# Performance work log

Hardware: AMD Instinct MI355X
Metric: run time of the kernel (lower is better)

## Reference

```python
import jax, jax.numpy as jnp
import numpy as np

N = 50000      # nodes
E = 800000     # edges
D = 128        # hidden dim (args.dim) == num_features
B = 5          # GIN blocks
G = 512        # graphs in batch
C = 10         # classes
EPS_GIN = 128.0  # GINConv(nn, in_channels) -> eps = in_channels = 128 (faithful to source)
BN_EPS = 1e-5


def setup_inputs() -> dict:
    key = jax.random.key(0)
    ks = jax.random.split(key, 12)
    xav = 0.1  # ~xavier_uniform std for 128x128
    x = jax.random.normal(ks[0], (N, D), jnp.float32)
    edge_index = jax.random.randint(ks[1], (2, E), 0, N, dtype=jnp.int64)
    batch = jax.random.randint(ks[2], (N,), 0, G, dtype=jnp.int64)
    return dict(
        x=x, edge_index=edge_index, batch=batch,
        W1=jax.random.normal(ks[3], (B, D, D), jnp.float32) * xav,
        b1=jnp.zeros((B, D), jnp.float32),
        g1=jnp.ones((B, D), jnp.float32),
        be1=jnp.zeros((B, D), jnp.float32),
        W2=jax.random.normal(ks[4], (B, D, D), jnp.float32) * xav,
        b2=jnp.zeros((B, D), jnp.float32),
        g2=jnp.ones((B, D), jnp.float32),
        be2=jnp.zeros((B, D), jnp.float32),
        bn_g=jnp.ones((B * D,), jnp.float32),
        bn_b=jnp.zeros((B * D,), jnp.float32),
        Wc1=jax.random.normal(ks[5], (B * D, D), jnp.float32) * 0.05,
        bc1=jnp.zeros((D,), jnp.float32),
        Wc2=jax.random.normal(ks[6], (D, C), jnp.float32) * 0.1,
        bc2=jnp.zeros((C,), jnp.float32),
    )


def _bn(h, g, b):
    # training-mode BatchNorm1d: biased variance over the batch (node/graph) dim
    mu = h.mean(axis=0)
    var = h.var(axis=0)
    return g * (h - mu) * jax.lax.rsqrt(var + BN_EPS) + b


def reference(x, edge_index, batch, W1, b1, g1, be1, W2, b2, g2, be2,
              bn_g, bn_b, Wc1, bc1, Wc2, bc2):
    src, dst = edge_index[0], edge_index[1]
    feats = []
    for i in range(B):
        # GIN aggregation: out[dst] += x[src]
        agg = jax.ops.segment_sum(x[src], dst, num_segments=N)   # [N, D]
        h = (1.0 + EPS_GIN) * x + agg
        h = _bn(jax.nn.relu(h @ W1[i] + b1[i]), g1[i], be1[i])
        h = _bn(jax.nn.relu(h @ W2[i] + b2[i]), g2[i], be2[i])
        x = h
        # global_add_pool per graph
        feats.append(jax.ops.segment_sum(x, batch, num_segments=G))  # [G, D]
    f = jnp.concatenate(feats, axis=1)          # [G, B*D]
    f = _bn(f, bn_g, bn_b)
    f = jax.nn.relu(f @ Wc1 + bc1)              # dropout p=0 (eval)
    logits = f @ Wc2 + bc2                      # [G, C]
    return jax.nn.log_softmax(logits, axis=-1)
```

## Files before the change

kernel.cpp:

```cpp
#include <hip/hip_runtime.h>
#include <hip/hip_bf16.h>

#define NN 50000
#define NE 800000
#define DD 128
#define NB 5
#define NG 512
#define NC 10
#define BN_EPS 1e-5f
#define EPS1 129.0f
#define GATHER_BLOCKS 12500

typedef __hip_bfloat16 bf16;
typedef __attribute__((ext_vector_type(8))) short short8;
typedef __attribute__((ext_vector_type(4))) float f32x4;

__device__ __forceinline__ float b2f(const bf16 v) { return __bfloat162float(v); }
__device__ __forceinline__ float us2f(unsigned int s) {
    return __uint_as_float((s & 0xffffu) << 16);
}
__device__ __forceinline__ unsigned pack2(float a, float b) {
    union { bf16 h; unsigned short u; } ua, ub;
    ua.h = __float2bfloat16(a); ub.h = __float2bfloat16(b);
    return ((unsigned)ub.u << 16) | (unsigned)ua.u;
}
__device__ __forceinline__ short f2bfs(float f) {
    union { bf16 h; short s; } u; u.h = __float2bfloat16(f); return u.s;
}

#define OFF_AGGH   0
#define OFF_XF     3200000
#define OFF_H1     6400000
#define OFF_FEATS  9600000
#define OFF_CSA    9927680
#define OFF_CSB    9927936
#define OFF_SC6    9928192
#define OFF_SH6    9928832
#define OFF_FLAGS  9929472
#define OFF_PARAMS 9929480
#define OFF_DEG    10055680
#define OFF_OFFS   10105680
#define OFF_ELIST  10155712
#define OFF_BDEG   10955712
#define OFF_BOFFS  10956224
#define OFF_RANK   10956800
#define OFF_PART   11006800

#define P_W1T  0
#define P_W2T  81920
#define P_WC1  163840
#define P_B1   245760
#define P_G1   246400
#define P_BE1  247040
#define P_B2   247680
#define P_G2   248320
#define P_BE2  248960
#define P_BNG  249600
#define P_BNB  250240
#define P_BC1  250880
#define P_WC2  251008
#define P_BC2  252288

struct SmallSrc { const void* s[11]; };

__global__ void k_detect(const unsigned* __restrict__ xw, const int* __restrict__ eiw,
                         const int* __restrict__ bw, int* flags, int* __restrict__ bdeg) {
    __shared__ int sh[3];
    const int t = threadIdx.x;
    bdeg[t] = 0; bdeg[256 + t] = 0;
    if (t < 3) sh[t] = 0;
    __syncthreads();
    int c = 0;
    for (int i = 0; i < 16; i++) {
        unsigned w = xw[t * 16 + i];
        unsigned e = (w >> 7) & 0xff;
        c += (e >= 110 && e <= 131) ? 1 : 0;
    }
    atomicAdd(&sh[0], c);
    atomicAdd(&sh[1], (eiw[2 * t + 1] != 0) ? 1 : 0);
    atomicAdd(&sh[2], (bw[2 * t + 1] != 0) ? 1 : 0);
    __syncthreads();
    if (t == 0) {
        flags[0] = (sh[0] > 2048) ? 1 : 0;
        flags[1] = (sh[1] < 8) ? 1 : 0;
        flags[2] = (sh[2] < 8) ? 1 : 0;
    }
}

__global__ void k_bhist(const int* __restrict__ flags, const int* __restrict__ batch,
                        int* __restrict__ bdeg, int* __restrict__ deg) {
    int n = blockIdx.x * 256 + threadIdx.x;
    if (n >= NN) return;
    deg[n] = 0;
    int g = flags[2] ? batch[2 * n] : batch[n];
    atomicAdd(&bdeg[g], 1);
}

__launch_bounds__(512)
__global__ void k_bscan(int* __restrict__ bdeg, int* __restrict__ boffs) {
    __shared__ int part[512];
    const int t = threadIdx.x;
    int d0 = bdeg[t];
    part[t] = d0;
    __syncthreads();
    for (int d = 1; d < 512; d <<= 1) {
        int v = (t >= d) ? part[t - d] : 0;
        __syncthreads();
        part[t] += v;
        __syncthreads();
    }
    int ex = part[t] - d0;
    boffs[t] = ex;
    bdeg[t] = ex;
    if (t == 511) boffs[512] = part[511];
}

__global__ void k_bplace(const int* __restrict__ flags, const int* __restrict__ batch,
                         int* __restrict__ bcur, int* __restrict__ rank) {
    int n = blockIdx.x * 256 + threadIdx.x;
    if (n >= NN) return;
    int g = flags[2] ? batch[2 * n] : batch[n];
    rank[n] = atomicAdd(&bcur[g], 1);
}

__global__ void k_convert_x(const int* __restrict__ flags, const void* __restrict__ xr,
                            const int* __restrict__ rank, bf16* __restrict__ xfh) {
    int i = blockIdx.x * 256 + threadIdx.x;
    int r = i >> 4, seg = i & 15;
    uint4 o;
    if (flags[0]) {
        o = ((const uint4*)xr)[i];
    } else {
        float4 a = ((const float4*)xr)[2 * i], b = ((const float4*)xr)[2 * i + 1];
        o.x = pack2(a.x, a.y); o.y = pack2(a.z, a.w);
        o.z = pack2(b.x, b.y); o.w = pack2(b.z, b.w);
    }
    ((uint4*)xfh)[(long)rank[r] * 16 + seg] = o;
}

__global__ void k_convert_params(const int* __restrict__ flags, const void* w1,
                                 const void* w2, const void* wc1, SmallSrc srcs,
                                 bf16* __restrict__ pb) {
    int i = blockIdx.x * 256 + threadIdx.x;
    if (i < 245760) {
        int which = i / 81920, j = i % 81920;
        const void* src = (which == 0) ? w1 : (which == 1) ? w2 : wc1;
        float v = flags[0] ? us2f(((const unsigned short*)src)[j]) : ((const float*)src)[j];
        if (which == 2) {
            pb[P_WC1 + j] = __float2bfloat16(v);
        } else {
            int layer = j >> 14, rem = j & 16383;
            int k = rem >> 7, c = rem & 127;
            bf16* dst = pb + (which == 0 ? P_W1T : P_W2T);
            dst[(layer << 14) + c * DD + k] = __float2bfloat16(v);
        }
    } else {
        int j = i - 245760;
        if (j >= 6538) return;
        int seg, off;
        if (j < 5120)      { seg = j / 640; off = j - seg * 640; }
        else if (j < 5248) { seg = 8;  off = j - 5120; }
        else if (j < 6528) { seg = 9;  off = j - 5248; }
        else               { seg = 10; off = j - 6528; }
        const void* s = srcs.s[seg];
        float v = flags[0] ? us2f(((const unsigned short*)s)[off]) : ((const float*)s)[off];
        pb[P_B1 + j] = __float2bfloat16(v);
    }
}

__global__ void k_hist(const int* __restrict__ flags, const int* __restrict__ ei,
                       const int* __restrict__ rank, int* __restrict__ deg) {
    int e = blockIdx.x * 256 + threadIdx.x;
    int d = flags[1] ? ei[2 * NE + 2 * e] : ei[NE + e];
    atomicAdd(&deg[rank[d]], 1);
}

__global__ void k_scan_part(const int* __restrict__ deg, int* __restrict__ part) {
    __shared__ int red[256];
    const int b = blockIdx.x, t = threadIdx.x;
    int i0 = b * 1024 + t * 4;
    int s = 0;
    if (i0 + 3 < NN) {
        int4 v = *(const int4*)(deg + i0);
        s = v.x + v.y + v.z + v.w;
    } else {
        for (int k = 0; k < 4; k++) if (i0 + k < NN) s += deg[i0 + k];
    }
    red[t] = s;
    __syncthreads();
    for (int d = 128; d > 0; d >>= 1) {
        if (t < d) red[t] += red[t + d];
        __syncthreads();
    }
    if (t == 0) part[b] = red[0];
}

__global__ void k_scan_apply(int* __restrict__ deg, const int* __restrict__ part,
                             int* __restrict__ offs) {
    __shared__ int red[256];
    __shared__ int base_sh, total_sh;
    const int b = blockIdx.x, t = threadIdx.x;
    if (t < 64) {
        int v = (t < 49) ? part[t] : 0;
        int s = v;
        for (int d = 1; d < 64; d <<= 1) {
            int x = __shfl_up(s, d);
            if (t >= d) s += x;
        }
        if (t == b)  base_sh = s - v;
        if (t == 48) total_sh = s;
    }
    int i0 = b * 1024 + t * 4;
    int v[4]; int s = 0;
    #pragma unroll
    for (int k = 0; k < 4; k++) {
        int idx = i0 + k;
        v[k] = (idx < NN) ? deg[idx] : 0;
        s += v[k];
    }
    red[t] = s;
    __syncthreads();
    for (int d = 1; d < 256; d <<= 1) {
        int x = (t >= d) ? red[t - d] : 0;
        __syncthreads();
        red[t] += x;
        __syncthreads();
    }
    if (b == 0 && t == 0) offs[NN] = total_sh;
    int pre = base_sh + ((t == 0) ? 0 : red[t - 1]);
    #pragma unroll
    for (int k = 0; k < 4; k++) {
        int idx = i0 + k;
        if (idx < NN) { offs[idx] = pre; deg[idx] = pre; pre += v[k]; }
    }
}

__global__ void k_place(const int* __restrict__ flags, const int* __restrict__ ei,
                        const int* __restrict__ rank, int* __restrict__ curs,
                        int* __restrict__ elist) {
    int e = blockIdx.x * 256 + threadIdx.x;
    int s, d;
    if (flags[1]) { s = ei[2 * e]; d = ei[2 * NE + 2 * e]; }
    else          { s = ei[e];     d = ei[NE + e]; }
    elist[atomicAdd(&curs[rank[d]], 1)] = rank[s];
}

__device__ __forceinline__ void pool_body(int g, int t, const bf16* __restrict__ xfh,
                                          const int* __restrict__ boffs,
                                          const float* __restrict__ csB,
                                          const bf16* __restrict__ g2,
                                          const bf16* __restrict__ be2,
                                          float* __restrict__ feats_blk) {
    __shared__ float2 red[3][64];
    const int l = t & 63;
    const int h = t >> 6;
    const int lo = boffs[g], hi = boffs[g + 1];
    const unsigned* xw = (const unsigned*)xfh;
    float s0 = 0.f, s1 = 0.f;
    for (int n = lo + h; n < hi; n += 4) {
        unsigned p = xw[(long)n * 64 + l];
        s0 += us2f(p); s1 += us2f(p >> 16);
    }
    if (h) red[h - 1][l] = make_float2(s0, s1);
    __syncthreads();
    if (h == 0) {
        s0 += red[0][l].x + red[1][l].x + red[2][l].x;
        s1 += red[0][l].y + red[1][l].y + red[2][l].y;
        int c = l * 2;
        float mu0 = csB[c] * (1.f / NN);
        float var0 = csB[128 + c] * (1.f / NN) - mu0 * mu0;
        float sc0 = b2f(g2[c]) * rsqrtf(var0 + BN_EPS);
        float sh0 = b2f(be2[c]) - mu0 * sc0;
        float mu1 = csB[c + 1] * (1.f / NN);
        float var1 = csB[128 + c + 1] * (1.f / NN) - mu1 * mu1;
        float sc1 = b2f(g2[c + 1]) * rsqrtf(var1 + BN_EPS);
        float sh1 = b2f(be2[c + 1]) - mu1 * sc1;
        float cnt = (float)(hi - lo);
        float* fp = feats_blk + (long)g * (NB * DD) + c;
        fp[0] = sc0 * s0 + cnt * sh0;
        fp[1] = sc1 * s1 + cnt * sh1;
    }
}

__global__ void k_gather_pool(const int* __restrict__ offs, const int* __restrict__ elist,
                              const bf16* __restrict__ xfh, bf16* __restrict__ aggh,
                              const float* __restrict__ csB, const bf16* __restrict__ g2,
                              const bf16* __restrict__ be2, float* __restrict__ csA_zero,
                              const int* __restrict__ boffs, float* __restrict__ feats_prev) {
    if (blockIdx.x >= GATHER_BLOCKS) {
        if (feats_prev)
            pool_body(blockIdx.x - GATHER_BLOCKS, threadIdx.x, xfh, boffs,
                      csB, g2, be2, feats_prev);
        return;
    }
    if (blockIdx.x == 0) csA_zero[threadIdx.x] = 0.f;
    const int w = threadIdx.x >> 6;
    const int lane = threadIdx.x & 63;
    const int n = blockIdx.x * 4 + w;
    const int base = offs[n], end = offs[n + 1];
    const unsigned* xw = (const unsigned*)xfh;
    unsigned sp = xw[(long)n * 64 + lane];
    float ax = EPS1 * us2f(sp), ay = EPS1 * us2f(sp >> 16);
    for (int i = base; i < end; i += 64) {
        int cnt = min(64, end - i);
        int e = (i + lane < end) ? elist[i + lane] : 0;
        int j = 0;
        for (; j + 16 <= cnt; j += 16) {
            unsigned p[16];
            #pragma unroll
            for (int q = 0; q < 16; q++) {
                int sj = __shfl(e, j + q);
                p[q] = xw[(long)sj * 64 + lane];
            }
            #pragma unroll
            for (int q = 0; q < 16; q++) {
                ax += us2f(p[q]); ay += us2f(p[q] >> 16);
            }
        }
        for (; j + 8 <= cnt; j += 8) {
            unsigned p[8];
            #pragma unroll
            for (int q = 0; q < 8; q++) {
                int sj = __shfl(e, j + q);
                p[q] = xw[(long)sj * 64 + lane];
            }
            #pragma unroll
            for (int q = 0; q < 8; q++) {
                ax += us2f(p[q]); ay += us2f(p[q] >> 16);
            }
        }
        for (; j < cnt; j++) {
            int sj = __shfl(e, j);
            unsigned p = xw[(long)sj * 64 + lane];
            ax += us2f(p); ay += us2f(p >> 16);
        }
    }
    if (csB) {
        int c = lane * 2;
        float fac = (float)(end - base) + EPS1;
        float mu0 = csB[c] * (1.f / NN);
        float var0 = csB[128 + c] * (1.f / NN) - mu0 * mu0;
        float sc0 = b2f(g2[c]) * rsqrtf(var0 + BN_EPS);
        float sh0 = b2f(be2[c]) - mu0 * sc0;
        float mu1 = csB[c + 1] * (1.f / NN);
        float var1 = csB[128 + c + 1] * (1.f / NN) - mu1 * mu1;
        float sc1 = b2f(g2[c + 1]) * rsqrtf(var1 + BN_EPS);
        float sh1 = b2f(be2[c + 1]) - mu1 * sc1;
        ax = sc0 * ax + fac * sh0;
        ay = sc1 * ay + fac * sh1;
    }
    ((unsigned*)aggh)[(long)n * 64 + lane] = pack2(ax, ay);
}

__launch_bounds__(256)
__global__ void k_pool(const bf16* __restrict__ xfh, const int* __restrict__ boffs,
                       const float* __restrict__ csB, const bf16* __restrict__ g2,
                       const bf16* __restrict__ be2, float* __restrict__ feats_blk) {
    pool_body(blockIdx.x, threadIdx.x, xfh, boffs, csB, g2, be2, feats_blk);
}

#define WS_S 136
__launch_bounds__(512)
__global__ void k_gemm_mfma(const bf16* __restrict__ A, const bf16* __restrict__ WT,
                            const bf16* __restrict__ bias,
                            const float* __restrict__ bn_cs, const bf16* __restrict__ bn_g,
                            const bf16* __restrict__ bn_be,
                            bf16* __restrict__ Out, float* __restrict__ cs_out,
                            float* cs_zero) {
    __shared__ short Ws[128 * WS_S];
    __shared__ float s_cs[256];
    __shared__ float s_sc[DD], s_sh[DD];
    const int t = threadIdx.x;
    const int row0 = blockIdx.x * 128;

    if (t < 256) {
        if (cs_zero && blockIdx.x == 0) cs_zero[t] = 0.f;
        s_cs[t] = 0.f;
    }
    if (bn_cs && t < DD) {
        float mu = bn_cs[t] * (1.f / NN);
        float var = bn_cs[128 + t] * (1.f / NN) - mu * mu;
        float sc = b2f(bn_g[t]) * rsqrtf(var + BN_EPS);
        s_sc[t] = sc;
        s_sh[t] = b2f(bn_be[t]) - mu * sc;
    }
    {
        const uint4* Wg = (const uint4*)WT;
        #pragma unroll
        for (int i = 0; i < 4; i++) {
            int idx = i * 512 + t;
            int row = idx >> 4, seg = idx & 15;
            *(uint4*)(&Ws[row * WS_S + seg * 8]) = Wg[idx];
        }
    }
    __syncthreads();

    const int w = t >> 6;
    const int lane = t & 63;
    const int m = lane & 15;
    const int half = lane >> 4;
    const int r = row0 + w * 16 + m;

    short8 afrag[4];
    if (r < NN) {
        #pragma unroll
        for (int kk = 0; kk < 4; kk++)
            afrag[kk] = *(const short8*)(A + (long)r * DD + kk * 32 + half * 8);
        if (bn_cs) {
            #pragma unroll
            for (int kk = 0; kk < 4; kk++) {
                int c0 = kk * 32 + half * 8;
                uint4 p = *(uint4*)&afrag[kk];
                float v0 = us2f(p.x) * s_sc[c0+0] + s_sh[c0+0];
                float v1 = us2f(p.x >> 16) * s_sc[c0+1] + s_sh[c0+1];
                float v2 = us2f(p.y) * s_sc[c0+2] + s_sh[c0+2];
                float v3 = us2f(p.y >> 16) * s_sc[c0+3] + s_sh[c0+3];
                float v4 = us2f(p.z) * s_sc[c0+4] + s_sh[c0+4];
                float v5 = us2f(p.z >> 16) * s_sc[c0+5] + s_sh[c0+5];
                float v6 = us2f(p.w) * s_sc[c0+6] + s_sh[c0+6];
                float v7 = us2f(p.w >> 16) * s_sc[c0+7] + s_sh[c0+7];
                p.x = pack2(v0, v1); p.y = pack2(v2, v3);
                p.z = pack2(v4, v5); p.w = pack2(v6, v7);
                afrag[kk] = *(short8*)&p;
            }
        }
    } else {
        #pragma unroll
        for (int kk = 0; kk < 4; kk++) afrag[kk] = (short8){0,0,0,0,0,0,0,0};
    }

    f32x4 acc[8];
    #pragma unroll
    for (int nt = 0; nt < 8; nt++) acc[nt] = (f32x4){0.f, 0.f, 0.f, 0.f};

    #pragma unroll
    for (int nt = 0; nt < 8; nt++) {
        const short* wrow = &Ws[(nt * 16 + m) * WS_S + half * 8];
        #pragma unroll
        for (int kk = 0; kk < 4; kk++) {
            short8 b = *(const short8*)(wrow + kk * 32);
            acc[nt] = __builtin_amdgcn_mfma_f32_16x16x32_bf16(afrag[kk], b, acc[nt], 0, 0, 0);
        }
    }

    __syncthreads();
    short* Cs = Ws;
    #pragma unroll
    for (int nt = 0; nt < 8; nt++) {
        int col = nt * 16 + m;
        float bi = b2f(bias[col]);
        float ps = 0.f, pq = 0.f;
        #pragma unroll
        for (int reg = 0; reg < 4; reg++) {
            int rr = row0 + w * 16 + half * 4 + reg;
            float o = fmaxf(acc[nt][reg] + bi, 0.f);
            Cs[(w * 16 + half * 4 + reg) * WS_S + col] = f2bfs(o);
            if (rr < NN) { ps += o; pq += o * o; }
        }
        ps += __shfl_xor(ps, 16); ps += __shfl_xor(ps, 32);
        pq += __shfl_xor(pq, 16); pq += __shfl_xor(pq, 32);
        if (half == 0) {
            atomicAdd(&s_cs[col], ps);
            atomicAdd(&s_cs[128 + col], pq);
        }
    }
    __syncthreads();
    #pragma unroll
    for (int i = 0; i < 4; i++) {
        int idx = i * 512 + t;
        int row = idx >> 4, seg = idx & 15;
        int rr = row0 + row;
        if (rr < NN)
            *(uint4*)(Out + (long)rr * DD + seg * 8) = *(uint4*)(&Cs[row * WS_S + seg * 8]);
    }
    if (t < 256) atomicAdd(&cs_out[t], s_cs[t]);
}

__global__ void k_feat_stats(const float* __restrict__ feats, const bf16* __restrict__ bn_g,
                             const bf16* __restrict__ bn_b, float* __restrict__ sc6,
                             float* __restrict__ sh6) {
    int j = blockIdx.x * 256 + threadIdx.x;
    if (j >= NB * DD) return;
    float s = 0.f, sq = 0.f;
    for (int g = 0; g < NG; g++) {
        float v = feats[(long)g * (NB * DD) + j];
        s += v; sq += v * v;
    }
    float mu = s / NG;
    float var = sq / NG - mu * mu;
    float sc = b2f(bn_g[j]) * rsqrtf(var + BN_EPS);
    sc6[j] = sc;
    sh6[j] = b2f(bn_b[j]) - mu * sc;
}

__launch_bounds__(128)
__global__ void k_head(const int* __restrict__ flags, const float* __restrict__ feats,
                       const float* __restrict__ sc6, const float* __restrict__ sh6,
                       const bf16* __restrict__ Wc1, const bf16* __restrict__ bc1,
                       const bf16* __restrict__ Wc2, const bf16* __restrict__ bc2,
                       void* out) {
    __shared__ float fs[NB * DD];
    __shared__ float f1[DD];
    __shared__ float lg[NC + 2];
    const int g = blockIdx.x, t = threadIdx.x;
    for (int j = t; j < NB * DD; j += 128)
        fs[j] = feats[(long)g * (NB * DD) + j] * sc6[j] + sh6[j];
    __syncthreads();
    float acc = b2f(bc1[t]);
    for (int j = 0; j < NB * DD; j++) acc += fs[j] * b2f(Wc1[j * DD + t]);
    f1[t] = fmaxf(acc, 0.f);
    __syncthreads();
    if (t < NC) {
        float a = b2f(bc2[t]);
        for (int k = 0; k < DD; k++) a += f1[k] * b2f(Wc2[k * NC + t]);
        lg[t] = a;
    }
    __syncthreads();
    if (t == 0) {
        float m = -1e30f;
        for (int c = 0; c < NC; c++) m = fmaxf(m, lg[c]);
        float s = 0.f;
        for (int c = 0; c < NC; c++) s += expf(lg[c] - m);
        lg[NC] = m + logf(s);
    }
    __syncthreads();
    if (t < NC) {
        float val = lg[t] - lg[NC];
        if (flags[0]) ((bf16*)out)[g * NC + t] = __float2bfloat16(val);
        else          ((float*)out)[g * NC + t] = val;
    }
}

extern "C" void kernel_launch(void* const* d_in, const int* in_sizes, int n_in,
                              void* d_out, int out_size, void* d_ws, size_t ws_size,
                              hipStream_t stream) {
    const void* x     = d_in[0];
    const int*  ei    = (const int*)d_in[1];
    const int*  batch = (const int*)d_in[2];

    float* ws    = (float*)d_ws;
    bf16*  aggh  = (bf16*)(ws + OFF_AGGH);
    bf16*  xfh   = (bf16*)(ws + OFF_XF);
    bf16*  h1h   = (bf16*)(ws + OFF_H1);
    float* feats = ws + OFF_FEATS;
    float* csA   = ws + OFF_CSA;
    float* csB   = ws + OFF_CSB;
    float* sc6   = ws + OFF_SC6;
    float* sh6   = ws + OFF_SH6;
    int*   flags = (int*)(ws + OFF_FLAGS);
    bf16*  pb    = (bf16*)(ws + OFF_PARAMS);
    int*   deg   = (int*)(ws + OFF_DEG);
    int*   offs  = (int*)(ws + OFF_OFFS);
    int*   elist = (int*)(ws + OFF_ELIST);
    int*   bdeg  = (int*)(ws + OFF_BDEG);
    int*   boffs = (int*)(ws + OFF_BOFFS);
    int*   rank  = (int*)(ws + OFF_RANK);
    int*   part  = (int*)(ws + OFF_PART);

    bf16 *pW1T = pb + P_W1T, *pW2T = pb + P_W2T, *pWc1 = pb + P_WC1;
    bf16 *pb1 = pb + P_B1, *pg1 = pb + P_G1, *pbe1 = pb + P_BE1;
    bf16 *pb2 = pb + P_B2, *pg2 = pb + P_G2, *pbe2 = pb + P_BE2;
    bf16 *pbng = pb + P_BNG, *pbnb = pb + P_BNB;
    bf16 *pbc1 = pb + P_BC1, *pWc2 = pb + P_WC2, *pbc2 = pb + P_BC2;

    k_detect<<<1, 256, 0, stream>>>((const unsigned*)x, ei, batch, flags, bdeg);

    k_bhist<<<(NN + 255) / 256, 256, 0, stream>>>(flags, batch, bdeg, deg);
    k_bscan<<<1, 512, 0, stream>>>(bdeg, boffs);
    k_bplace<<<(NN + 255) / 256, 256, 0, stream>>>(flags, batch, bdeg, rank);

    k_convert_x<<<NN * DD / 8 / 256, 256, 0, stream>>>(flags, x, rank, xfh);

    SmallSrc ss;
    ss.s[0] = d_in[4];  ss.s[1] = d_in[5];  ss.s[2] = d_in[6];
    ss.s[3] = d_in[8];  ss.s[4] = d_in[9];  ss.s[5] = d_in[10];
    ss.s[6] = d_in[11]; ss.s[7] = d_in[12];
    ss.s[8] = d_in[14]; ss.s[9] = d_in[15]; ss.s[10] = d_in[16];
    k_convert_params<<<(245760 + 6538 + 255) / 256, 256, 0, stream>>>(
        flags, d_in[3], d_in[7], d_in[13], ss, pb);

    k_hist<<<NE / 256, 256, 0, stream>>>(flags, ei, rank, deg);
    k_scan_part<<<49, 256, 0, stream>>>(deg, part);
    k_scan_apply<<<49, 256, 0, stream>>>(deg, part, offs);
    k_place<<<NE / 256, 256, 0, stream>>>(flags, ei, rank, deg, elist);

    const int gemm_blocks = (NN + 127) / 128;
    for (int i = 0; i < NB; i++) {
        k_gather_pool<<<GATHER_BLOCKS + NG, 256, 0, stream>>>(
            offs, elist, xfh, aggh,
            (i == 0) ? nullptr : csB,
            pg2 + (i - 1) * DD, pbe2 + (i - 1) * DD, csA,
            boffs, (i == 0) ? nullptr : feats + (i - 1) * DD);
        k_gemm_mfma<<<gemm_blocks, 512, 0, stream>>>(aggh, pW1T + i * DD * DD, pb1 + i * DD,
                                                     nullptr, nullptr, nullptr,
                                                     h1h, csA, csB);
        k_gemm_mfma<<<gemm_blocks, 512, 0, stream>>>(h1h, pW2T + i * DD * DD, pb2 + i * DD,
                                                     csA, pg1 + i * DD, pbe1 + i * DD,
                                                     xfh, csB, nullptr);
    }
    k_pool<<<NG, 256, 0, stream>>>(xfh, boffs, csB, pg2 + (NB - 1) * DD,
                                   pbe2 + (NB - 1) * DD, feats + (NB - 1) * DD);

    k_feat_stats<<<3, 256, 0, stream>>>(feats, pbng, pbnb, sc6, sh6);
    k_head<<<NG, 128, 0, stream>>>(flags, feats, sc6, sh6, pWc1, pbc1, pWc2, pbc2, d_out);
}
```

Before: 685.2 us.

## Fuse GEMM pair and tail kernels using grid-wide software barriers

Merges the two per-block GEMM launches into one persistent kernel of 512 blocks that synchronizes on a global atomic barrier between the two layers. The final pool, feature-stats and head kernels are merged the same way, and the edge histogram is folded into the x-convert launch. The aim is to cut kernel launch gaps and drain/fill overhead. In exchange it relies on all 512 blocks being co-resident; if they are not, the spin barrier deadlocks.

```diff
diff --git a/kernel.cpp b/kernel.cpp
--- a/kernel.cpp
+++ b/kernel.cpp
@@ -10,6 +10,8 @@
 #define BN_EPS 1e-5f
 #define EPS1 129.0f
 #define GATHER_BLOCKS 12500
+#define GP_BLOCKS 512
+#define GEMM_TILES 391
 
 typedef __hip_bfloat16 bf16;
 typedef __attribute__((ext_vector_type(8))) short short8;
@@ -26,6 +28,22 @@
 }
 __device__ __forceinline__ short f2bfs(float f) {
     union { bf16 h; short s; } u; u.h = __float2bfloat16(f); return u.s;
+}
+
+__device__ __forceinline__ void gbar(int* cnt, int* gen, int nb) {
+    __syncthreads();
+    if (threadIdx.x == 0) {
+        __threadfence();
+        int g = atomicAdd(gen, 0);
+        if (atomicAdd(cnt, 1) == nb - 1) {
+            atomicExch(cnt, 0);
+            atomicAdd(gen, 1);
+        } else {
+            while (atomicAdd(gen, 0) == g) __builtin_amdgcn_s_sleep(2);
+        }
+        __threadfence();
+    }
+    __syncthreads();
 }
 
 #define OFF_AGGH   0
@@ -45,6 +63,7 @@
 #define OFF_BOFFS  10956224
 #define OFF_RANK   10956800
 #define OFF_PART   11006800
+#define OFF_BAR    11006864
 
 #define P_W1T  0
 #define P_W2T  81920
@@ -97,9 +116,11 @@
 }
 
 __launch_bounds__(512)
-__global__ void k_bscan(int* __restrict__ bdeg, int* __restrict__ boffs) {
+__global__ void k_bscan(int* __restrict__ bdeg, int* __restrict__ boffs,
+                        int* __restrict__ barst) {
     __shared__ int part[512];
     const int t = threadIdx.x;
+    if (t < 4) barst[t] = 0;
     int d0 = bdeg[t];
     part[t] = d0;
     __syncthreads();
@@ -123,8 +144,15 @@
     rank[n] = atomicAdd(&bcur[g], 1);
 }
 
-__global__ void k_convert_x(const int* __restrict__ flags, const void* __restrict__ xr,
-                            const int* __restrict__ rank, bf16* __restrict__ xfh) {
+__global__ void k_convert_hist(const int* __restrict__ flags, const void* __restrict__ xr,
+                               const int* __restrict__ rank, bf16* __restrict__ xfh,
+                               const int* __restrict__ ei, int* __restrict__ deg) {
+    if (blockIdx.x >= 3125) {
+        int e = (blockIdx.x - 3125) * 256 + threadIdx.x;
+        int d = flags[1] ? ei[2 * NE + 2 * e] : ei[NE + e];
+        atomicAdd(&deg[rank[d]], 1);
+        return;
+    }
     int i = blockIdx.x * 256 + threadIdx.x;
     int r = i >> 4, seg = i & 15;
     uint4 o;
@@ -166,13 +194,6 @@
         float v = flags[0] ? us2f(((const unsigned short*)s)[off]) : ((const float*)s)[off];
         pb[P_B1 + j] = __float2bfloat16(v);
     }
-}
-
-__global__ void k_hist(const int* __restrict__ flags, const int* __restrict__ ei,
-                       const int* __restrict__ rank, int* __restrict__ deg) {
-    int e = blockIdx.x * 256 + threadIdx.x;
-    int d = flags[1] ? ei[2 * NE + 2 * e] : ei[NE + e];
-    atomicAdd(&deg[rank[d]], 1);
 }
 
 __global__ void k_scan_part(const int* __restrict__ deg, int* __restrict__ part) {
@@ -280,6 +301,7 @@
         fp[0] = sc0 * s0 + cnt * sh0;
         fp[1] = sc1 * s1 + cnt * sh1;
     }
+    __syncthreads();
 }
 
 __global__ void k_gather_pool(const int* __restrict__ offs, const int* __restrict__ elist,
@@ -352,38 +374,17 @@
     ((unsigned*)aggh)[(long)n * 64 + lane] = pack2(ax, ay);
 }
 
-__launch_bounds__(256)
-__global__ void k_pool(const bf16* __restrict__ xfh, const int* __restrict__ boffs,
-                       const float* __restrict__ csB, const bf16* __restrict__ g2,
-                       const bf16* __restrict__ be2, float* __restrict__ feats_blk) {
-    pool_body(blockIdx.x, threadIdx.x, xfh, boffs, csB, g2, be2, feats_blk);
-}
-
 #define WS_S 136
-__launch_bounds__(512)
-__global__ void k_gemm_mfma(const bf16* __restrict__ A, const bf16* __restrict__ WT,
-                            const bf16* __restrict__ bias,
-                            const float* __restrict__ bn_cs, const bf16* __restrict__ bn_g,
-                            const bf16* __restrict__ bn_be,
-                            bf16* __restrict__ Out, float* __restrict__ cs_out,
-                            float* cs_zero) {
-    __shared__ short Ws[128 * WS_S];
-    __shared__ float s_cs[256];
-    __shared__ float s_sc[DD], s_sh[DD];
-    const int t = threadIdx.x;
-    const int row0 = blockIdx.x * 128;
-
-    if (t < 256) {
-        if (cs_zero && blockIdx.x == 0) cs_zero[t] = 0.f;
-        s_cs[t] = 0.f;
-    }
-    if (bn_cs && t < DD) {
-        float mu = bn_cs[t] * (1.f / NN);
-        float var = bn_cs[128 + t] * (1.f / NN) - mu * mu;
-        float sc = b2f(bn_g[t]) * rsqrtf(var + BN_EPS);
-        s_sc[t] = sc;
-        s_sh[t] = b2f(bn_be[t]) - mu * sc;
-    }
+__device__ __forceinline__ void gemm_tile(const bf16* __restrict__ A,
+                                          const bf16* __restrict__ WT,
+                                          const bf16* __restrict__ bias,
+                                          const float* __restrict__ s_sc,
+                                          const float* __restrict__ s_sh, bool do_bn,
+                                          bf16* __restrict__ Out,
+                                          float* __restrict__ cs_out,
+                                          short* Ws, float* s_cs, int tile, int t) {
+    const int row0 = tile * 128;
+    if (t < 256) s_cs[t] = 0.f;
     {
         const uint4* Wg = (const uint4*)WT;
         #pragma unroll
@@ -406,7 +407,7 @@
         #pragma unroll
         for (int kk = 0; kk < 4; kk++)
             afrag[kk] = *(const short8*)(A + (long)r * DD + kk * 32 + half * 8);
-        if (bn_cs) {
+        if (do_bn) {
             #pragma unroll
             for (int kk = 0; kk < 4; kk++) {
                 int c0 = kk * 32 + half * 8;
@@ -474,41 +475,87 @@
             *(uint4*)(Out + (long)rr * DD + seg * 8) = *(uint4*)(&Cs[row * WS_S + seg * 8]);
     }
     if (t < 256) atomicAdd(&cs_out[t], s_cs[t]);
-}
-
-__global__ void k_feat_stats(const float* __restrict__ feats, const bf16* __restrict__ bn_g,
-                             const bf16* __restrict__ bn_b, float* __restrict__ sc6,
-                             float* __restrict__ sh6) {
-    int j = blockIdx.x * 256 + threadIdx.x;
-    if (j >= NB * DD) return;
-    float s = 0.f, sq = 0.f;
-    for (int g = 0; g < NG; g++) {
-        float v = feats[(long)g * (NB * DD) + j];
-        s += v; sq += v * v;
-    }
-    float mu = s / NG;
-    float var = sq / NG - mu * mu;
-    float sc = b2f(bn_g[j]) * rsqrtf(var + BN_EPS);
-    sc6[j] = sc;
-    sh6[j] = b2f(bn_b[j]) - mu * sc;
-}
-
-__launch_bounds__(128)
-__global__ void k_head(const int* __restrict__ flags, const float* __restrict__ feats,
-                       const float* __restrict__ sc6, const float* __restrict__ sh6,
+    __syncthreads();
+}
+
+__launch_bounds__(512)
+__global__ void k_gemm_pair(const bf16* __restrict__ aggh, bf16* __restrict__ h1h,
+                            bf16* __restrict__ xfh,
+                            const bf16* __restrict__ W1T, const bf16* __restrict__ b1,
+                            const bf16* __restrict__ W2T, const bf16* __restrict__ b2,
+                            const bf16* __restrict__ g1, const bf16* __restrict__ be1,
+                            float* __restrict__ csA, float* __restrict__ csB,
+                            int* __restrict__ barst) {
+    __shared__ short Ws[128 * WS_S];
+    __shared__ float s_cs[256];
+    __shared__ float s_sc[DD], s_sh[DD];
+    const int t = threadIdx.x;
+    const int bid = blockIdx.x;
+
+    if (bid == 400 && t < 256) csB[t] = 0.f;
+    if (bid < GEMM_TILES)
+        gemm_tile(aggh, W1T, b1, nullptr, nullptr, false, h1h, csA, Ws, s_cs, bid, t);
+
+    gbar(&barst[0], &barst[1], GP_BLOCKS);
+
+    if (t < DD) {
+        float mu = csA[t] * (1.f / NN);
+        float var = csA[128 + t] * (1.f / NN) - mu * mu;
+        float sc = b2f(g1[t]) * rsqrtf(var + BN_EPS);
+        s_sc[t] = sc;
+        s_sh[t] = b2f(be1[t]) - mu * sc;
+    }
+    __syncthreads();
+    if (bid < GEMM_TILES)
+        gemm_tile(h1h, W2T, b2, s_sc, s_sh, true, xfh, csB, Ws, s_cs, bid, t);
+}
+
+__launch_bounds__(256)
+__global__ void k_tail(const int* __restrict__ flags, const bf16* __restrict__ xfh,
+                       const int* __restrict__ boffs, const float* __restrict__ csB,
+                       const bf16* __restrict__ g2, const bf16* __restrict__ be2,
+                       float* __restrict__ feats, const bf16* __restrict__ bn_g,
+                       const bf16* __restrict__ bn_b, float* __restrict__ sc6,
+                       float* __restrict__ sh6,
                        const bf16* __restrict__ Wc1, const bf16* __restrict__ bc1,
                        const bf16* __restrict__ Wc2, const bf16* __restrict__ bc2,
-                       void* out) {
+                       void* out, int* __restrict__ barst) {
+    const int t = threadIdx.x, bid = blockIdx.x;
+
+    pool_body(bid, t, xfh, boffs, csB, g2, be2, feats + (NB - 1) * DD);
+
+    gbar(&barst[2], &barst[3], GP_BLOCKS);
+
+    {
+        int j = bid * 256 + t;
+        if (j < NB * DD) {
+            float s = 0.f, sq = 0.f;
+            for (int g = 0; g < NG; g++) {
+                float v = feats[(long)g * (NB * DD) + j];
+                s += v; sq += v * v;
+            }
+            float mu = s / NG;
+            float var = sq / NG - mu * mu;
+            float sc = b2f(bn_g[j]) * rsqrtf(var + BN_EPS);
+            sc6[j] = sc;
+            sh6[j] = b2f(bn_b[j]) - mu * sc;
+        }
+    }
+
+    gbar(&barst[2], &barst[3], GP_BLOCKS);
+
     __shared__ float fs[NB * DD];
     __shared__ float f1[DD];
     __shared__ float lg[NC + 2];
-    const int g = blockIdx.x, t = threadIdx.x;
-    for (int j = t; j < NB * DD; j += 128)
+    const int g = bid;
+    for (int j = t; j < NB * DD; j += 256)
         fs[j] = feats[(long)g * (NB * DD) + j] * sc6[j] + sh6[j];
     __syncthreads();
-    float acc = b2f(bc1[t]);
-    for (int j = 0; j < NB * DD; j++) acc += fs[j] * b2f(Wc1[j * DD + t]);
-    f1[t] = fmaxf(acc, 0.f);
+    if (t < DD) {
+        float acc = b2f(bc1[t]);
+        for (int j = 0; j < NB * DD; j++) acc += fs[j] * b2f(Wc1[j * DD + t]);
+        f1[t] = fmaxf(acc, 0.f);
+    }
     __syncthreads();
     if (t < NC) {
         float a = b2f(bc2[t]);
@@ -556,6 +603,7 @@
     int*   boffs = (int*)(ws + OFF_BOFFS);
     int*   rank  = (int*)(ws + OFF_RANK);
     int*   part  = (int*)(ws + OFF_PART);
+    int*   barst = (int*)(ws + OFF_BAR);
 
     bf16 *pW1T = pb + P_W1T, *pW2T = pb + P_W2T, *pWc1 = pb + P_WC1;
     bf16 *pb1 = pb + P_B1, *pg1 = pb + P_G1, *pbe1 = pb + P_BE1;
@@ -564,12 +612,11 @@
     bf16 *pbc1 = pb + P_BC1, *pWc2 = pb + P_WC2, *pbc2 = pb + P_BC2;
 
     k_detect<<<1, 256, 0, stream>>>((const unsigned*)x, ei, batch, flags, bdeg);
-
     k_bhist<<<(NN + 255) / 256, 256, 0, stream>>>(flags, batch, bdeg, deg);
-    k_bscan<<<1, 512, 0, stream>>>(bdeg, boffs);
+    k_bscan<<<1, 512, 0, stream>>>(bdeg, boffs, barst);
     k_bplace<<<(NN + 255) / 256, 256, 0, stream>>>(flags, batch, bdeg, rank);
 
-    k_convert_x<<<NN * DD / 8 / 256, 256, 0, stream>>>(flags, x, rank, xfh);
+    k_convert_hist<<<6250, 256, 0, stream>>>(flags, x, rank, xfh, ei, deg);
 
     SmallSrc ss;
     ss.s[0] = d_in[4];  ss.s[1] = d_in[5];  ss.s[2] = d_in[6];
@@ -579,28 +626,26 @@
     k_convert_params<<<(245760 + 6538 + 255) / 256, 256, 0, stream>>>(
         flags, d_in[3], d_in[7], d_in[13], ss, pb);
 
-    k_hist<<<NE / 256, 256, 0, stream>>>(flags, ei, rank, deg);
     k_scan_part<<<49, 256, 0, stream>>>(deg, part);
     k_scan_apply<<<49, 256, 0, stream>>>(deg, part, offs);
     k_place<<<NE / 256, 256, 0, stream>>>(flags, ei, rank, deg, elist);
 
-    const int gemm_blocks = (NN + 127) / 128;
     for (int i = 0; i < NB; i++) {
         k_gather_pool<<<GATHER_BLOCKS + NG, 256, 0, stream>>>(
             offs, elist, xfh, aggh,
             (i == 0) ? nullptr : csB,
             pg2 + (i - 1) * DD, pbe2 + (i - 1) * DD, csA,
             boffs, (i == 0) ? nullptr : feats + (i - 1) * DD);
-        k_gemm_mfma<<<gemm_blocks, 512, 0, stream>>>(aggh, pW1T + i * DD * DD, pb1 + i * DD,
-                                                     nullptr, nullptr, nullptr,
-                                                     h1h, csA, csB);
-        k_gemm_mfma<<<gemm_blocks, 512, 0, stream>>>(h1h, pW2T + i * DD * DD, pb2 + i * DD,
-                                                     csA, pg1 + i * DD, pbe1 + i * DD,
-                                                     xfh, csB, nullptr);
-    }
-    k_pool<<<NG, 256, 0, stream>>>(xfh, boffs, csB, pg2 + (NB - 1) * DD,
-                                   pbe2 + (NB - 1) * DD, feats + (NB - 1) * DD);
-
-    k_feat_stats<<<3, 256, 0, stream>>>(feats, pbng, pbnb, sc6, sh6);
-    k_head<<<NG, 128, 0, stream>>>(flags, feats, sc6, sh6, pWc1, pbc1, pWc2, pbc2, d_out);
-}
+        k_gemm_pair<<<GP_BLOCKS, 512, 0, stream>>>(
+            aggh, h1h, xfh,
+            pW1T + i * DD * DD, pb1 + i * DD,
+            pW2T + i * DD * DD, pb2 + i * DD,
+            pg1 + i * DD, pbe1 + i * DD,
+            csA, csB, barst);
+    }
+
+    k_tail<<<GP_BLOCKS, 256, 0, stream>>>(flags, xfh, boffs, csB,
+                                          pg2 + (NB - 1) * DD, pbe2 + (NB - 1) * DD,
+                                          feats, pbng, pbnb, sc6, sh6,
+                                          pWc1, pbc1, pWc2, pbc2, d_out, barst);
+}
```

Result: slower. 1.010 ms (+47.4%).
